# Performance work log

Hardware: AMD Instinct MI355X
Metric: run time of the kernel (lower is better)

## Reference

```python
import jax, jax.numpy as jnp
import numpy as np

N_NODES = 65536
N_EDGES = 1048576
IN_FEATS = 128
H1 = 128
H2 = 256
N_CLASSES = 16


def setup_inputs() -> dict:
    key = jax.random.key(0)
    ks = jax.random.split(key, 12)
    s = 0.05
    x = jax.random.normal(ks[0], (N_NODES, IN_FEATS), dtype=jnp.float32)
    src = jax.random.randint(ks[1], (N_EDGES,), 0, N_NODES, dtype=jnp.int32)
    dst = jax.random.randint(ks[2], (N_EDGES,), 0, N_NODES, dtype=jnp.int32)
    # SAGEConv('pool') params: fc_pool (bias), fc_self (no bias), fc_neigh (no bias), output bias
    Wp = jax.random.normal(ks[3], (H1, IN_FEATS), dtype=jnp.float32) * s
    bp = jnp.zeros((H1,), dtype=jnp.float32)
    Ws = jax.random.normal(ks[4], (H1, IN_FEATS), dtype=jnp.float32) * s
    Wn = jax.random.normal(ks[5], (H1, H1), dtype=jnp.float32) * s
    bn = jnp.zeros((H1,), dtype=jnp.float32)
    # MLP head
    W1 = jax.random.normal(ks[6], (H2, H1), dtype=jnp.float32) * s
    b1 = jnp.zeros((H2,), dtype=jnp.float32)
    W2 = jax.random.normal(ks[7], (N_CLASSES, H2), dtype=jnp.float32) * s
    b2 = jnp.zeros((N_CLASSES,), dtype=jnp.float32)
    return {"x": x, "Wp": Wp, "bp": bp, "Ws": Ws, "Wn": Wn, "bn": bn,
            "W1": W1, "b1": b1, "W2": W2, "b2": b2, "src": src, "dst": dst}


def reference(x, Wp, bp, Ws, Wn, bn, W1, b1, W2, b2, src, dst):
    N = x.shape[0]
    # SAGEConv 'pool': per-edge MLP on gathered source features, segment-max over dst
    m = jax.nn.relu(x[src] @ Wp.T + bp)              # [E, H1]
    pooled = jax.ops.segment_max(m, dst, num_segments=N)  # [N, H1], -inf for isolated
    pooled = jnp.where(jnp.isneginf(pooled), 0.0, pooled)
    h = x @ Ws.T + pooled @ Wn.T + bn                # combine self + neigh
    h = jax.nn.leaky_relu(h)                         # slope 0.01 matches torch default
    h = jax.nn.leaky_relu(h @ W1.T + b1)
    # dropout is identity in eval mode
    h = jax.nn.sigmoid(h @ W2.T + b2)
    return h
```

## Files before the change

### kernel.cpp

```cpp
#include <hip/hip_runtime.h>
#include <cstdint>
#include <cstddef>

typedef __attribute__((ext_vector_type(8))) __bf16 bf16x8;
typedef __attribute__((ext_vector_type(4))) float f32x4;

union bf8pack { unsigned short u[8]; bf16x8 v; uint4 q; };

#define BCAP 768

static __device__ __forceinline__ unsigned short f2b(float f) {
    union { float f; unsigned int u; } v; v.f = f;
    unsigned int u = v.u;
    unsigned int r = (u + 0x7fffu + ((u >> 16) & 1u)) >> 16;
    return (unsigned short)r;
}

static __device__ __forceinline__ bf16x8 cvt8(const float* __restrict__ p) {
    float4 f0 = *(const float4*)p;
    float4 f1 = *(const float4*)(p + 4);
    bf8pack pk;
    pk.u[0] = f2b(f0.x); pk.u[1] = f2b(f0.y);
    pk.u[2] = f2b(f0.z); pk.u[3] = f2b(f0.w);
    pk.u[4] = f2b(f1.x); pk.u[5] = f2b(f1.y);
    pk.u[6] = f2b(f1.z); pk.u[7] = f2b(f1.w);
    return pk.v;
}

__global__ __launch_bounds__(256) void mega0(
    const int* __restrict__ src, const int* __restrict__ dst,
    int* __restrict__ bcnt, unsigned int* __restrict__ pairs,
    const float* __restrict__ x, const float* __restrict__ Wp,
    const float* __restrict__ bp,
    const float* __restrict__ Ws, const float* __restrict__ Wn,
    const float* __restrict__ W1, const float* __restrict__ W2,
    unsigned short* __restrict__ Wcat, unsigned short* __restrict__ W1_b,
    unsigned short* __restrict__ W2_b, unsigned short* __restrict__ y)
{
    const int tid = threadIdx.x;
    const int bx = (int)blockIdx.x;

    if (bx >= 768) {
        int i = (bx - 768) * 256 + tid;
        if (i < 32768) {
            int o = i >> 8, k = i & 255;
            Wcat[i] = f2b(k < 128 ? Ws[o * 128 + k] : Wn[o * 128 + (k - 128)]);
        } else if (i < 65536) {
            W1_b[i - 32768] = f2b(W1[i - 32768]);
        } else {
            W2_b[i - 65536] = f2b(W2[i - 65536]);
        }
        return;
    }

    if (bx >= 256) {
        const int bm = bx - 256;
        const int w  = tid >> 6;
        const int wm = w & 1, wn = w >> 1;
        const int l  = tid & 63;
        const int lr = l & 15, quad = l >> 4;
        const int m0 = bm * 128 + wm * 64;
        const int n0 = wn * 64;

        f32x4 acc[4][4];
#pragma unroll
        for (int i = 0; i < 4; i++)
#pragma unroll
            for (int j = 0; j < 4; j++) acc[i][j] = (f32x4){0.f, 0.f, 0.f, 0.f};

        const float* Apf = x  + (size_t)(m0 + lr) * 128 + quad * 8;
        const float* Bpf = Wp + (size_t)(n0 + lr) * 128 + quad * 8;

#pragma unroll
        for (int ks = 0; ks < 4; ks++) {
            bf16x8 af[4], bf[4];
#pragma unroll
            for (int i = 0; i < 4; i++)
                af[i] = cvt8(Apf + (size_t)i * 16 * 128 + ks * 32);
#pragma unroll
            for (int i = 0; i < 4; i++)
                bf[i] = cvt8(Bpf + (size_t)i * 16 * 128 + ks * 32);
#pragma unroll
            for (int mi = 0; mi < 4; mi++)
#pragma unroll
                for (int ni = 0; ni < 4; ni++)
                    acc[mi][ni] = __builtin_amdgcn_mfma_f32_16x16x32_bf16(
                        af[mi], bf[ni], acc[mi][ni], 0, 0, 0);
        }

#pragma unroll
        for (int ni = 0; ni < 4; ni++) {
            const int col = n0 + ni * 16 + lr;
            const float bv = bp[col];
#pragma unroll
            for (int mi = 0; mi < 4; mi++) {
#pragma unroll
                for (int r = 0; r < 4; r++) {
                    const int row = m0 + mi * 16 + quad * 4 + r;
                    float v = acc[mi][ni][r] + bv;
                    v = v > 0.f ? v : 0.f;
                    y[(size_t)row * 128 + col] = f2b(v);
                }
            }
        }
        return;
    }

    __shared__ int h[2048];
    __shared__ int base_l[2048];
    __shared__ int cnt[2048];
    for (int i = tid; i < 2048; i += 256) { h[i] = 0; cnt[i] = 0; }
    __syncthreads();
    const int base = bx * 4096;
    int d_r[16], s_r[16];
    const int4* s4 = (const int4*)(src + base);
    const int4* d4 = (const int4*)(dst + base);
#pragma unroll
    for (int i = 0; i < 4; i++) {
        int4 dv = d4[tid + i * 256];
        int4 sv = s4[tid + i * 256];
        d_r[i * 4 + 0] = dv.x; d_r[i * 4 + 1] = dv.y;
        d_r[i * 4 + 2] = dv.z; d_r[i * 4 + 3] = dv.w;
        s_r[i * 4 + 0] = sv.x; s_r[i * 4 + 1] = sv.y;
        s_r[i * 4 + 2] = sv.z; s_r[i * 4 + 3] = sv.w;
    }
#pragma unroll
    for (int i = 0; i < 16; i++)
        atomicAdd(&h[((unsigned)d_r[i]) >> 5], 1);
    __syncthreads();
    for (int i = tid; i < 2048; i += 256)
        base_l[i] = h[i] ? (i * BCAP + atomicAdd(&bcnt[i], h[i])) : 0;
    __syncthreads();
#pragma unroll
    for (int i = 0; i < 16; i++) {
        int b = ((unsigned)d_r[i]) >> 5;
        int pos = base_l[b] + atomicAdd(&cnt[b], 1);
        if (pos < (b + 1) * BCAP)
            pairs[pos] = ((unsigned)s_r[i] << 5) | ((unsigned)d_r[i] & 31u);
    }
}

__global__ __launch_bounds__(256) void bucket_pool3(
    const unsigned int* __restrict__ yu, const int* __restrict__ bcnt,
    const unsigned int* __restrict__ pairs, unsigned short* __restrict__ pooled)
{
    __shared__ unsigned short ldsSrc[1024];
    __shared__ int bin[32], offl[32], cnt2[32];
    const int b = blockIdx.x;
    const int tid = threadIdx.x;
    if (tid < 32) { bin[tid] = 0; cnt2[tid] = 0; }
    __syncthreads();
    const int beg = b * BCAP;
    int nb = bcnt[b]; nb = nb < BCAP ? nb : BCAP;

    for (int i = tid; i < nb; i += 256)
        atomicAdd(&bin[pairs[beg + i] & 31u], 1);
    __syncthreads();
    if (tid == 0) {
        int run = 0;
        for (int i = 0; i < 32; i++) { offl[i] = run; run += bin[i]; }
    }
    __syncthreads();
    for (int i = tid; i < nb; i += 256) {
        unsigned int p = pairs[beg + i];
        int d = p & 31u;
        int slot = offl[d] + atomicAdd(&cnt2[d], 1);
        ldsSrc[slot] = (unsigned short)(p >> 5);
    }
    __syncthreads();

    const int w = tid >> 6, lane = tid & 63;
    for (int ni = 0; ni < 8; ni++) {
        const int n = w * 8 + ni;
        const int e0 = offl[n], cnt = bin[n];
        float ax = 0.f, ay = 0.f;
        for (int e = 0; e < cnt; e += 8) {
            int s[8]; unsigned int v[8];
#pragma unroll
            for (int j = 0; j < 8; j++) {
                int idx = e + j; idx = idx < cnt ? idx : cnt - 1;
                s[j] = ldsSrc[e0 + idx];
            }
#pragma unroll
            for (int j = 0; j < 8; j++) v[j] = yu[(size_t)s[j] * 64 + lane];
#pragma unroll
            for (int j = 0; j < 8; j++) {
                ax = fmaxf(ax, __uint_as_float(v[j] << 16));
                ay = fmaxf(ay, __uint_as_float(v[j] & 0xffff0000u));
            }
        }
        unsigned int packed = (__float_as_uint(ax) >> 16) | (__float_as_uint(ay) & 0xffff0000u);
        ((unsigned int*)pooled)[(size_t)(b * 32 + n) * 64 + lane] = packed;
    }
}

__global__ __launch_bounds__(256, 6) void k45(
    const float* __restrict__ x, const unsigned short* __restrict__ pooled,
    const unsigned short* __restrict__ Wcat, const float* __restrict__ bn,
    const unsigned short* __restrict__ W1_b, const float* __restrict__ b1,
    const unsigned short* __restrict__ W2_b, const float* __restrict__ b2,
    float* __restrict__ out)
{
    __shared__ unsigned short S[32 * 264];
    const int tid = threadIdx.x;
    const int w = tid >> 6, l = tid & 63;
    const int lr = l & 15, quad = l >> 4;
    const int row0 = blockIdx.x * 32;

    {
        f32x4 acc[2][2];
#pragma unroll
        for (int i = 0; i < 2; i++)
#pragma unroll
            for (int j = 0; j < 2; j++) acc[i][j] = (f32x4){0.f, 0.f, 0.f, 0.f};

        const float* Axp = x + (size_t)(row0 + lr) * 128 + quad * 8;
        const unsigned short* App = pooled + (size_t)(row0 + lr) * 128 + quad * 8;
        const unsigned short* Bp = Wcat + (size_t)(w * 32 + lr) * 256 + quad * 8;

#pragma unroll
        for (int ks = 0; ks < 8; ks++) {
            bf16x8 af[2], bf[2];
            if (ks < 4) {
#pragma unroll
                for (int i = 0; i < 2; i++)
                    af[i] = cvt8(Axp + (size_t)i * 16 * 128 + ks * 32);
            } else {
#pragma unroll
                for (int i = 0; i < 2; i++)
                    af[i] = *(const bf16x8*)(App + (size_t)i * 16 * 128 + (ks - 4) * 32);
            }
#pragma unroll
            for (int i = 0; i < 2; i++)
                bf[i] = *(const bf16x8*)(Bp + (size_t)i * 16 * 256 + ks * 32);
#pragma unroll
            for (int mi = 0; mi < 2; mi++)
#pragma unroll
                for (int ni = 0; ni < 2; ni++)
                    acc[mi][ni] = __builtin_amdgcn_mfma_f32_16x16x32_bf16(
                        af[mi], bf[ni], acc[mi][ni], 0, 0, 0);
        }

#pragma unroll
        for (int ni = 0; ni < 2; ni++) {
            const int col = w * 32 + ni * 16 + lr;
            const float bv = bn[col];
#pragma unroll
            for (int mi = 0; mi < 2; mi++) {
#pragma unroll
                for (int r = 0; r < 4; r++) {
                    const int row = mi * 16 + quad * 4 + r;
                    float v = acc[mi][ni][r] + bv;
                    v = v > 0.f ? v : 0.01f * v;
                    S[row * 136 + col] = f2b(v);
                }
            }
        }
    }
    __syncthreads();

    {
        f32x4 acc[2][4];
#pragma unroll
        for (int i = 0; i < 2; i++)
#pragma unroll
            for (int j = 0; j < 4; j++) acc[i][j] = (f32x4){0.f, 0.f, 0.f, 0.f};

        const unsigned short* Bp = W1_b + (size_t)(w * 64 + lr) * 128 + quad * 8;

#pragma unroll
        for (int ks = 0; ks < 4; ks++) {
            bf16x8 af[2], bfr[4];
#pragma unroll
            for (int i = 0; i < 2; i++)
                af[i] = *(const bf16x8*)&S[(i * 16 + lr) * 136 + ks * 32 + quad * 8];
#pragma unroll
            for (int i = 0; i < 4; i++)
                bfr[i] = *(const bf16x8*)(Bp + (size_t)i * 16 * 128 + ks * 32);
#pragma unroll
            for (int mi = 0; mi < 2; mi++)
#pragma unroll
                for (int ni = 0; ni < 4; ni++)
                    acc[mi][ni] = __builtin_amdgcn_mfma_f32_16x16x32_bf16(
                        af[mi], bfr[ni], acc[mi][ni], 0, 0, 0);
        }
        __syncthreads();

#pragma unroll
        for (int ni = 0; ni < 4; ni++) {
            const int col = w * 64 + ni * 16 + lr;
            const float bv = b1[col];
#pragma unroll
            for (int mi = 0; mi < 2; mi++) {
#pragma unroll
                for (int r = 0; r < 4; r++) {
                    const int row = mi * 16 + quad * 4 + r;
                    float v = acc[mi][ni][r] + bv;
                    v = v > 0.f ? v : 0.01f * v;
                    S[row * 264 + col] = f2b(v);
                }
            }
        }
    }
    __syncthreads();

    if (w < 2) {
        const int m0 = w * 16;
        f32x4 a2 = (f32x4){0.f, 0.f, 0.f, 0.f};
#pragma unroll
        for (int ks = 0; ks < 8; ks++) {
            bf16x8 a = *(const bf16x8*)&S[(m0 + lr) * 264 + ks * 32 + quad * 8];
            bf16x8 bb = *(const bf16x8*)(W2_b + (size_t)lr * 256 + ks * 32 + quad * 8);
            a2 = __builtin_amdgcn_mfma_f32_16x16x32_bf16(a, bb, a2, 0, 0, 0);
        }
        const float bv = b2[lr];
#pragma unroll
        for (int r = 0; r < 4; r++) {
            const int row = row0 + m0 + quad * 4 + r;
            float v = a2[r] + bv;
            out[(size_t)row * 16 + lr] = 1.f / (1.f + __expf(-v));
        }
    }
}

extern "C" void kernel_launch(void* const* d_in, const int* in_sizes, int n_in,
                              void* d_out, int out_size, void* d_ws, size_t ws_size,
                              hipStream_t stream)
{
    const float* x  = (const float*)d_in[0];
    const float* Wp = (const float*)d_in[1];
    const float* bp = (const float*)d_in[2];
    const float* Ws = (const float*)d_in[3];
    const float* Wn = (const float*)d_in[4];
    const float* bn = (const float*)d_in[5];
    const float* W1 = (const float*)d_in[6];
    const float* b1 = (const float*)d_in[7];
    const float* W2 = (const float*)d_in[8];
    const float* b2 = (const float*)d_in[9];
    const int* src  = (const int*)d_in[10];
    const int* dst  = (const int*)d_in[11];
    float* out = (float*)d_out;

    const int N = in_sizes[0] / 128;

    unsigned short* y      = (unsigned short*)d_ws;
    unsigned short* pooled = (unsigned short*)((char*)d_ws + (size_t)16 * 1024 * 1024);
    unsigned short* Wcat   = (unsigned short*)((char*)d_ws + (size_t)32 * 1024 * 1024);
    unsigned short* W1_b = Wcat + 32768;
    unsigned short* W2_b = W1_b + 32768;
    int* bcnt = (int*)(W2_b + 4096);
    unsigned int* pairs = (unsigned int*)(bcnt + 2048);

    dim3 blk(256);

    hipMemsetAsync(bcnt, 0, 2048 * sizeof(int), stream);

    mega0<<<1040, blk, 0, stream>>>(src, dst, bcnt, pairs,
                                    x, Wp, bp, Ws, Wn, W1, W2,
                                    Wcat, W1_b, W2_b, y);

    bucket_pool3<<<2048, blk, 0, stream>>>((const unsigned int*)y, bcnt, pairs, pooled);

    k45<<<N / 32, blk, 0, stream>>>(x, pooled, Wcat, bn, W1_b, b1, W2_b, b2, out);
}
```

Measured before the change: 221.1 us.

## Fuse bucket max-pooling into the combine/MLP kernel via swizzled LDS tile

Merges the bucket segment-max kernel and the dense combine+MLP kernel into one kernel. Each block now pools its 32 destination nodes straight into a shared-memory tile with an XOR swizzle, then reads the pooled A-fragments from LDS instead of a global pooled buffer. This drops a kernel launch and the global write and read of the pooled matrix. In exchange the block uses more LDS, gets a lower occupancy bound (4 instead of 6), and can no longer overlap the gather-heavy phase with the MFMA phase across separate kernels.

Measured after the change: 209.0 us. 5.5% less time.

```diff
diff --git a/kernel.cpp b/kernel.cpp
--- a/kernel.cpp
+++ b/kernel.cpp
@@ -140,14 +140,26 @@
     }
 }
 
-__global__ __launch_bounds__(256) void bucket_pool3(
+__global__ __launch_bounds__(256, 4) void megaB(
     const unsigned int* __restrict__ yu, const int* __restrict__ bcnt,
-    const unsigned int* __restrict__ pairs, unsigned short* __restrict__ pooled)
+    const unsigned int* __restrict__ pairs,
+    const float* __restrict__ x,
+    const unsigned short* __restrict__ Wcat, const float* __restrict__ bn,
+    const unsigned short* __restrict__ W1_b, const float* __restrict__ b1,
+    const unsigned short* __restrict__ W2_b, const float* __restrict__ b2,
+    float* __restrict__ out)
 {
+    __shared__ unsigned short S[32 * 264];
     __shared__ unsigned short ldsSrc[1024];
     __shared__ int bin[32], offl[32], cnt2[32];
+    unsigned int* PS = (unsigned int*)&S[32 * 136];
+
     const int b = blockIdx.x;
     const int tid = threadIdx.x;
+    const int w = tid >> 6, l = tid & 63;
+    const int lr = l & 15, quad = l >> 4;
+    const int row0 = b * 32;
+
     if (tid < 32) { bin[tid] = 0; cnt2[tid] = 0; }
     __syncthreads();
     const int beg = b * BCAP;
@@ -169,7 +181,6 @@
     }
     __syncthreads();
 
-    const int w = tid >> 6, lane = tid & 63;
     for (int ni = 0; ni < 8; ni++) {
         const int n = w * 8 + ni;
         const int e0 = offl[n], cnt = bin[n];
@@ -182,7 +193,7 @@
                 s[j] = ldsSrc[e0 + idx];
             }
 #pragma unroll
-            for (int j = 0; j < 8; j++) v[j] = yu[(size_t)s[j] * 64 + lane];
+            for (int j = 0; j < 8; j++) v[j] = yu[(size_t)s[j] * 64 + l];
 #pragma unroll
             for (int j = 0; j < 8; j++) {
                 ax = fmaxf(ax, __uint_as_float(v[j] << 16));
@@ -190,22 +201,9 @@
             }
         }
         unsigned int packed = (__float_as_uint(ax) >> 16) | (__float_as_uint(ay) & 0xffff0000u);
-        ((unsigned int*)pooled)[(size_t)(b * 32 + n) * 64 + lane] = packed;
-    }
-}
-
-__global__ __launch_bounds__(256, 6) void k45(
-    const float* __restrict__ x, const unsigned short* __restrict__ pooled,
-    const unsigned short* __restrict__ Wcat, const float* __restrict__ bn,
-    const unsigned short* __restrict__ W1_b, const float* __restrict__ b1,
-    const unsigned short* __restrict__ W2_b, const float* __restrict__ b2,
-    float* __restrict__ out)
-{
-    __shared__ unsigned short S[32 * 264];
-    const int tid = threadIdx.x;
-    const int w = tid >> 6, l = tid & 63;
-    const int lr = l & 15, quad = l >> 4;
-    const int row0 = blockIdx.x * 32;
+        PS[n * 64 + (l ^ ((n & 7) << 2))] = packed;
+    }
+    __syncthreads();
 
     {
         f32x4 acc[2][2];
@@ -215,7 +213,6 @@
             for (int j = 0; j < 2; j++) acc[i][j] = (f32x4){0.f, 0.f, 0.f, 0.f};
 
         const float* Axp = x + (size_t)(row0 + lr) * 128 + quad * 8;
-        const unsigned short* App = pooled + (size_t)(row0 + lr) * 128 + quad * 8;
         const unsigned short* Bp = Wcat + (size_t)(w * 32 + lr) * 256 + quad * 8;
 
 #pragma unroll
@@ -227,8 +224,11 @@
                     af[i] = cvt8(Axp + (size_t)i * 16 * 128 + ks * 32);
             } else {
 #pragma unroll
-                for (int i = 0; i < 2; i++)
-                    af[i] = *(const bf16x8*)(App + (size_t)i * 16 * 128 + (ks - 4) * 32);
+                for (int i = 0; i < 2; i++) {
+                    const int row = i * 16 + lr;
+                    const int c0 = (ks - 4) * 16 + quad * 4;
+                    af[i] = *(const bf16x8*)&PS[row * 64 + (c0 ^ ((row & 7) << 2))];
+                }
             }
 #pragma unroll
             for (int i = 0; i < 2; i++)
@@ -343,9 +343,8 @@
 
     const int N = in_sizes[0] / 128;
 
-    unsigned short* y      = (unsigned short*)d_ws;
-    unsigned short* pooled = (unsigned short*)((char*)d_ws + (size_t)16 * 1024 * 1024);
-    unsigned short* Wcat   = (unsigned short*)((char*)d_ws + (size_t)32 * 1024 * 1024);
+    unsigned short* y    = (unsigned short*)d_ws;
+    unsigned short* Wcat = (unsigned short*)((char*)d_ws + (size_t)16 * 1024 * 1024);
     unsigned short* W1_b = Wcat + 32768;
     unsigned short* W2_b = W1_b + 32768;
     int* bcnt = (int*)(W2_b + 4096);
@@ -359,7 +358,6 @@
                                     x, Wp, bp, Ws, Wn, W1, W2,
                                     Wcat, W1_b, W2_b, y);
 
-    bucket_pool3<<<2048, blk, 0, stream>>>((const unsigned int*)y, bcnt, pairs, pooled);
-
-    k45<<<N / 32, blk, 0, stream>>>(x, pooled, Wcat, bn, W1_b, b1, W2_b, b2, out);
-}
+    megaB<<<N / 32, blk, 0, stream>>>((const unsigned int*)y, bcnt, pairs,
+                                      x, Wcat, bn, W1_b, b1, W2_b, b2, out);
+}
```
